# Performance work log

Measured on AMD Instinct MI355X. Metric: run time of the kernel, lower is better.

The kernel has to match this reference:

```python
import jax, jax.numpy as jnp
import numpy as np

S1 = (42, 1600, 1408); S2 = (21, 800, 704); S3 = (11, 400, 352); S4 = (6, 200, 176)
OFF = np.array([[dz, dy, dx] for dz in (-1, 0, 1) for dy in (-1, 0, 1) for dx in (-1, 0, 1)], np.int64)
KOFF = np.array([[kz, ky, kx] for kz in (0, 1, 2) for ky in (0, 1, 2) for kx in (0, 1, 2)], np.int64)

def _keys(c, s):
    return (c[:, 0] * s[1] + c[:, 1]) * s[2] + c[:, 2]

def _lookup(skeys, qk, valid):
    pos = np.searchsorted(skeys, qk)
    posc = np.clip(pos, 0, len(skeys) - 1)
    found = valid & (skeys[posc] == qk)
    return np.where(found, posc, -1).astype(np.int32)

def _subm_nbr(coords, skeys, shape):
    N = len(coords); nbr = np.empty((N, 27), np.int32); sh = np.array(shape)
    for t in range(27):
        q = coords + OFF[t]
        valid = np.all((q >= 0) & (q < sh), axis=1)
        nbr[:, t] = _lookup(skeys, _keys(q, shape), valid)
    return nbr

def _inv_nbr(fcoords, ckeys, cshape):
    # inverse of stride-2, pad-1, k-3 sparse conv: coarse = (fine + 1 - k) / 2
    N = len(fcoords); nbr = np.empty((N, 27), np.int32); csh = np.array(cshape)
    for t in range(27):
        cand = fcoords + 1 - KOFF[t]
        valid = np.all(cand >= 0, axis=1) & np.all(cand % 2 == 0, axis=1)
        cc = cand // 2
        valid &= np.all(cc < csh, axis=1)
        nbr[:, t] = _lookup(ckeys, _keys(cc, cshape), valid)
    return nbr

def _geometry():
    rng = np.random.default_rng(0)
    n = 130000
    c = np.stack([rng.integers(0, S1[i], n) for i in range(3)], 1).astype(np.int64)
    uk, idx = np.unique(_keys(c, S1), return_index=True)
    c1 = c[idx][:100000]; k1 = uk[:len(c1)]
    def down(cf, s):
        cc = cf // 2
        uk, idx = np.unique(_keys(cc, s), return_index=True)
        return cc[idx], uk
    c2, k2 = down(c1, S2); c3, k3 = down(c2, S3); c4, k4 = down(c3, S4)
    return dict(nbr4=_subm_nbr(c4, k4, S4), inv43=_inv_nbr(c3, k4, S4),
                nbr3=_subm_nbr(c3, k3, S3), inv32=_inv_nbr(c2, k3, S3),
                nbr2=_subm_nbr(c2, k2, S2), inv21=_inv_nbr(c1, k2, S2),
                nbr1=_subm_nbr(c1, k1, S1), n4=len(c4), n1=len(c1))

_SPECS = [("m4", 64, 64), ("i4", 64, 64), ("m3", 64, 64), ("i3", 64, 32),
          ("m2", 32, 32), ("i2", 32, 16), ("m1", 16, 16), ("c5", 16, 3)]

def _params(key):
    p = {}
    for i, (nm, ci, co) in enumerate(_SPECS):
        k = jax.random.fold_in(key, i)
        p["W_" + nm] = jax.random.normal(k, (27, ci, co), jnp.float32) * (1.0 / np.sqrt(27.0 * ci))
        p["g_" + nm] = jnp.ones((co,), jnp.float32)
        p["b_" + nm] = jnp.zeros((co,), jnp.float32)
    return p

def setup_inputs() -> dict:
    geo = _geometry()
    key = jax.random.key(0)
    inp = {k: jnp.asarray(v) for k, v in geo.items() if k.startswith(("nbr", "inv"))}
    inp["x"] = jax.random.normal(jax.random.fold_in(key, 100), (geo["n4"], 64), jnp.float32)
    inp.update(_params(key))
    return inp

def _block(f, nbr, W, g, b, relu=True):
    # gather-GEMM (sparse conv), then BatchNorm1d (training mode, eps=1e-3), then ReLU
    m = nbr >= 0                                             # [N,27]
    x = jnp.where(m[..., None], f[jnp.maximum(nbr, 0)], 0.0)  # [N,27,Cin]
    y = jnp.einsum('nkc,kcd->nd', x, W)                      # [N,Cout]
    mu = y.mean(0); var = y.var(0)
    y = (y - mu) * jax.lax.rsqrt(var + 1e-3) * g + b
    return jax.nn.relu(y) if relu else y

def reference(x, nbr4, inv43, nbr3, inv32, nbr2, inv21, nbr1,
              W_m4, g_m4, b_m4, W_i4, g_i4, b_i4, W_m3, g_m3, b_m3, W_i3, g_i3, b_i3,
              W_m2, g_m2, b_m2, W_i2, g_i2, b_i2, W_m1, g_m1, b_m1, W_c5, g_c5, b_c5):
    h = _block(x, nbr4, W_m4, g_m4, b_m4)      # subm4: [N4,64]
    h = _block(h, inv43, W_i4, g_i4, b_i4)     # inverse conv4 -> [N3,64]
    h = _block(h, nbr3, W_m3, g_m3, b_m3)      # subm3
    h = _block(h, inv32, W_i3, g_i3, b_i3)     # inverse conv3 -> [N2,32]
    h = _block(h, nbr2, W_m2, g_m2, b_m2)      # subm2
    h = _block(h, inv21, W_i2, g_i2, b_i2)     # inverse conv2 -> [N1,16]
    h = _block(h, nbr1, W_m1, g_m1, b_m1)      # subm1
    return _block(h, nbr1, W_c5, g_c5, b_c5, relu=False)  # conv5 (shares subm1 rulebook), BN only
```

## Files before the change

kernel.cpp:

```cpp
#include <hip/hip_runtime.h>

typedef _Float16 HALF;
typedef _Float16 f16x8 __attribute__((ext_vector_type(8)));
typedef float f32x4 __attribute__((ext_vector_type(4)));
typedef int i32x4 __attribute__((ext_vector_type(4)));

struct WArgs { const float* W[8]; HALF* dst[8]; };

__global__ void convert_all_w_kernel(WArgs a)
{
    const int CIs[8]  = {64, 64, 64, 64, 32, 32, 16, 16};
    const int COs[8]  = {64, 64, 64, 32, 32, 16, 16, 3};
    const int COPs[8] = {64, 64, 64, 32, 32, 16, 16, 16};
    const int L = blockIdx.y;
    const int CI = CIs[L], CO = COs[L], COP = COPs[L];
    const int K = 27 * CI, KP = (K + 31) & ~31;
    const int total = COP * KP;
    for (int i = blockIdx.x * 256 + threadIdx.x; i < total; i += gridDim.x * 256) {
        int jp = i / KP;
        int kp = i - jp * KP;
        float v = (jp < CO && kp < K) ? a.W[L][(size_t)kp * CO + jp] : 0.f;
        a.dst[L][((size_t)(kp >> 5) * COP + jp) * 32 + (kp & 31)] = (HALF)v;
    }
}

__global__ void convert_x_kernel(const float* __restrict__ x, HALF* __restrict__ xh, int total)
{
    int i = blockIdx.x * 256 + threadIdx.x;
    if (i < total) xh[i] = (HALF)x[i];
}

template<int CI, int CO_PAD, int NMT, bool FUSED>
__global__ __launch_bounds__(256, 2) void conv_kernel(
    const HALF* __restrict__ h, const int* __restrict__ nbr,
    const HALF* __restrict__ Wt, HALF* __restrict__ yout,
    float* __restrict__ sums, int n,
    const float* __restrict__ psums, const float* __restrict__ pg,
    const float* __restrict__ pb, float pinvn)
{
    constexpr int K    = 27 * CI;
    constexpr int KP   = (K + 31) & ~31;
    constexpr int NCH  = KP / 32;
    constexpr int NJB  = CO_PAD / 16;
    constexpr int NW   = 4;
    constexpr int NCB  = (CI >= 64) ? 2 : 1;
    constexpr int LOG2CI = (CI == 64) ? 6 : ((CI == 32) ? 5 : 4);

    __shared__ float red[2][NW][CO_PAD];

    const int wv   = threadIdx.x >> 6;
    const int lane = threadIdx.x & 63;
    const int l15  = lane & 15;
    const int lq   = lane >> 4;

    int bid = blockIdx.x;
    {
        const int nwg = gridDim.x;
        const int q = nwg >> 3, r = nwg & 7;
        const int xcd = bid & 7, idx = bid >> 3;
        bid = (xcd < r ? xcd * (q + 1) : r * (q + 1) + (xcd - r) * q) + idx;
    }
    const int waveRow = bid * (NW * 16 * NMT) + wv * (16 * NMT);

    f32x4 acc[NMT][NJB];
#pragma unroll
    for (int mt = 0; mt < NMT; ++mt)
#pragma unroll
        for (int jb = 0; jb < NJB; ++jb)
#pragma unroll
            for (int r = 0; r < 4; ++r) acc[mt][jb][r] = 0.f;

    int  nbo[NMT];
    bool rok[NMT];
#pragma unroll
    for (int mt = 0; mt < NMT; ++mt) {
        const int row = waveRow + mt * 16 + l15;
        rok[mt] = row < n;
        nbo[mt] = min(row, n - 1) * 27;
    }

    f16x8 sc8[NCB], bi8[NCB];
    if constexpr (FUSED) {
#pragma unroll
        for (int cb = 0; cb < NCB; ++cb) {
            const int c0 = cb * 32 + ((lq * 8) & (CI - 1));
#pragma unroll
            for (int j = 0; j < 8; ++j) {
                const int c = c0 + j;
                const float mu  = psums[c] * pinvn;
                const float var = psums[CI + c] * pinvn - mu * mu;
                const float sc  = rsqrtf(var + 1e-3f) * pg[c];
                sc8[cb][j] = (HALF)sc;
                bi8[cb][j] = (HALF)(pb[c] - mu * sc);
            }
        }
    }

    #define TAPOF(kc) ((CI == 16) ? (2 * (kc) + (lq >> 1)) : ((CI == 64) ? ((kc) >> 1) : (kc)))
    #define CHOF(kc)  (((kc) * 32 + lq * 8) & (CI - 1))

    int   ipf[2][NMT];
    f16x8 apf[2][NMT];
#pragma unroll
    for (int p = 0; p < 2; ++p) {
#pragma unroll
        for (int mt = 0; mt < NMT; ++mt) {
            const int t   = TAPOF(p);
            const int v   = nbr[nbo[mt] + (t < 27 ? t : 26)];
            const int idx = (rok[mt] && t < 27) ? v : -1;
            ipf[p][mt] = idx;
            apf[p][mt] = *(const f16x8*)(h + ((max(idx, 0) << LOG2CI) + CHOF(p)));
        }
    }

#pragma unroll
    for (int kc = 0; kc < NCH; ++kc) {
        const int cur = kc & 1;
        const int ccb = (NCB == 2) ? (kc & 1) : 0;

        const HALF* wb = Wt + (size_t)kc * (CO_PAD * 32) + lq * 8;
        f16x8 b[NJB];
#pragma unroll
        for (int jb = 0; jb < NJB; ++jb)
            b[jb] = *(const f16x8*)(wb + (size_t)(jb * 16 + l15) * 32);

        f16x8 a_use[NMT];
        int   i_use[NMT];
#pragma unroll
        for (int mt = 0; mt < NMT; ++mt) { a_use[mt] = apf[cur][mt]; i_use[mt] = ipf[cur][mt]; }

        if (kc + 2 < NCH) {
#pragma unroll
            for (int mt = 0; mt < NMT; ++mt) {
                const int t   = TAPOF(kc + 2);
                const int v   = nbr[nbo[mt] + (t < 27 ? t : 26)];
                const int idx = (rok[mt] && t < 27) ? v : -1;
                ipf[cur][mt] = idx;
                apf[cur][mt] = *(const f16x8*)(h + ((max(idx, 0) << LOG2CI) + CHOF(kc + 2)));
            }
        }

#pragma unroll
        for (int mt = 0; mt < NMT; ++mt) {
            f16x8 a = a_use[mt];
            if constexpr (FUSED) {
                a = a * sc8[ccb] + bi8[ccb];
#pragma unroll
                for (int j = 0; j < 8; ++j)
                    a[j] = (a[j] < (HALF)0.f) ? (HALF)0.f : a[j];
            }
            const int m = ~(i_use[mt] >> 31);
            i32x4 ai = __builtin_bit_cast(i32x4, a);
            ai.x &= m; ai.y &= m; ai.z &= m; ai.w &= m;
            a = __builtin_bit_cast(f16x8, ai);
#pragma unroll
            for (int jb = 0; jb < NJB; ++jb)
                acc[mt][jb] = __builtin_amdgcn_mfma_f32_16x16x32_f16(a, b[jb], acc[mt][jb], 0, 0, 0);
        }
    }
    #undef TAPOF
    #undef CHOF

#pragma unroll
    for (int jb = 0; jb < NJB; ++jb) {
        const int col = jb * 16 + l15;
        float s = 0.f, sq = 0.f;
#pragma unroll
        for (int mt = 0; mt < NMT; ++mt) {
            const int rb = waveRow + mt * 16 + lq * 4;
#pragma unroll
            for (int r = 0; r < 4; ++r) {
                if (rb + r < n) {
                    const float v = acc[mt][jb][r];
                    yout[(size_t)(rb + r) * CO_PAD + col] = (HALF)v;
                    s += v;
                    sq += v * v;
                }
            }
        }
        s  += __shfl_xor(s, 16);  s  += __shfl_xor(s, 32);
        sq += __shfl_xor(sq, 16); sq += __shfl_xor(sq, 32);
        if (lane < 16) { red[0][wv][col] = s; red[1][wv][col] = sq; }
    }
    __syncthreads();
    if (threadIdx.x < CO_PAD) {
        float s = 0.f, sq = 0.f;
#pragma unroll
        for (int w = 0; w < NW; ++w) { s += red[0][w][threadIdx.x]; sq += red[1][w][threadIdx.x]; }
        atomicAdd(&sums[threadIdx.x], s);
        atomicAdd(&sums[CO_PAD + threadIdx.x], sq);
    }
}

__global__ void bn_out_kernel(const HALF* __restrict__ y, const float* __restrict__ sums,
                              const float* __restrict__ g, const float* __restrict__ b,
                              int n, float invn, float* __restrict__ out)
{
    int i = blockIdx.x * 256 + threadIdx.x;
    if (i >= n * 3) return;
    int row = i / 3;
    int c = i - row * 3;
    float mu  = sums[c] * invn;
    float var = sums[16 + c] * invn - mu * mu;
    float sc  = rsqrtf(var + 1e-3f) * g[c];
    out[i] = ((float)y[(size_t)row * 16 + c] - mu) * sc + b[c];
}

extern "C" void kernel_launch(void* const* d_in, const int* in_sizes, int n_in,
                              void* d_out, int out_size, void* d_ws, size_t ws_size,
                              hipStream_t stream)
{
    const int* nbr4  = (const int*)d_in[0];
    const int* inv43 = (const int*)d_in[1];
    const int* nbr3  = (const int*)d_in[2];
    const int* inv32 = (const int*)d_in[3];
    const int* nbr2  = (const int*)d_in[4];
    const int* inv21 = (const int*)d_in[5];
    const int* nbr1  = (const int*)d_in[6];
    const float* x   = (const float*)d_in[7];

    const int n4 = in_sizes[0] / 27;
    const int n3 = in_sizes[1] / 27;
    const int n2 = in_sizes[3] / 27;
    const int n1 = in_sizes[5] / 27;

    const int CIs[8]  = {64, 64, 64, 64, 32, 32, 16, 16};
    const int COPs[8] = {64, 64, 64, 32, 32, 16, 16, 16};
    int KPs[8], wtoff[8];
    int wtot = 0;
    for (int s = 0; s < 8; ++s) {
        KPs[s] = ((27 * CIs[s] + 31) / 32) * 32;
        wtoff[s] = wtot;
        wtot += COPs[s] * KPs[s];
    }

    char* ws = (char*)d_ws;
    HALF* wt = (HALF*)ws;
    size_t off = ((size_t)wtot * sizeof(HALF) + 255) & ~(size_t)255;
    float* sums = (float*)(ws + off);
    off += 8 * 128 * sizeof(float);
    off = (off + 255) & ~(size_t)255;
    HALF* xh = (HALF*)(ws + off);
    off += ((size_t)n4 * 64 * sizeof(HALF) + 255) & ~(size_t)255;
    size_t bufElems = 0;
    {
        size_t cand[4] = {(size_t)n4 * 64, (size_t)n3 * 64, (size_t)n2 * 32, (size_t)n1 * 16};
        for (int i = 0; i < 4; ++i) if (cand[i] > bufElems) bufElems = cand[i];
    }
    HALF* Y0 = (HALF*)(ws + off);
    off += (bufElems * sizeof(HALF) + 255) & ~(size_t)255;
    HALF* Y1 = (HALF*)(ws + off);

    hipMemsetAsync(sums, 0, 8 * 128 * sizeof(float), stream);

    WArgs wa;
    for (int s = 0; s < 8; ++s) { wa.W[s] = (const float*)d_in[8 + 3 * s]; wa.dst[s] = wt + wtoff[s]; }
    {
        int maxTotal = 64 * KPs[0];
        dim3 grid((maxTotal + 255) / 256, 8);
        convert_all_w_kernel<<<grid, 256, 0, stream>>>(wa);
    }
    convert_x_kernel<<<(n4 * 64 + 255) / 256, 256, 0, stream>>>(x, xh, n4 * 64);

#define G(s) ((const float*)d_in[9 + 3 * (s)])
#define B(s) ((const float*)d_in[10 + 3 * (s)])
#define SUMS(s) (sums + (s) * 128)
#define GRID(nn) (((nn) + 127) / 128)

    conv_kernel<64, 64, 2, false><<<GRID(n4), 256, 0, stream>>>(
        xh, nbr4, wt + wtoff[0], Y0, SUMS(0), n4, nullptr, nullptr, nullptr, 0.f);
    conv_kernel<64, 64, 2, true><<<GRID(n3), 256, 0, stream>>>(
        Y0, inv43, wt + wtoff[1], Y1, SUMS(1), n3, SUMS(0), G(0), B(0), 1.f / n4);
    conv_kernel<64, 64, 2, true><<<GRID(n3), 256, 0, stream>>>(
        Y1, nbr3, wt + wtoff[2], Y0, SUMS(2), n3, SUMS(1), G(1), B(1), 1.f / n3);
    conv_kernel<64, 32, 2, true><<<GRID(n2), 256, 0, stream>>>(
        Y0, inv32, wt + wtoff[3], Y1, SUMS(3), n2, SUMS(2), G(2), B(2), 1.f / n3);
    conv_kernel<32, 32, 2, true><<<GRID(n2), 256, 0, stream>>>(
        Y1, nbr2, wt + wtoff[4], Y0, SUMS(4), n2, SUMS(3), G(3), B(3), 1.f / n2);
    conv_kernel<32, 16, 2, true><<<GRID(n1), 256, 0, stream>>>(
        Y0, inv21, wt + wtoff[5], Y1, SUMS(5), n1, SUMS(4), G(4), B(4), 1.f / n2);
    conv_kernel<16, 16, 2, true><<<GRID(n1), 256, 0, stream>>>(
        Y1, nbr1, wt + wtoff[6], Y0, SUMS(6), n1, SUMS(5), G(5), B(5), 1.f / n1);
    conv_kernel<16, 16, 2, true><<<GRID(n1), 256, 0, stream>>>(
        Y0, nbr1, wt + wtoff[7], Y1, SUMS(7), n1, SUMS(6), G(6), B(6), 1.f / n1);
    bn_out_kernel<<<(n1 * 3 + 255) / 256, 256, 0, stream>>>(
        Y1, SUMS(7), G(7), B(7), n1, 1.f / n1, (float*)d_out);

#undef G
#undef B
#undef SUMS
#undef GRID
}
```

Measured before the change: 568.1 us.

## Split K reduction across waves and shard BN stat atomics per XCD

Each block now covers 32 rows instead of 128. Its four waves each take a quarter of the K chunks for the same rows, and the partial accumulators are combined through a tree reduction in shared memory before wave 0 writes the output and statistics. The BN sums are spread across 8 slices chosen by XCD, so atomics contend less, and consumers add up the 8 slices when they compute mean and variance. This raises the number of blocks and the parallelism per row at the cost of extra LDS traffic, three barriers, and reloading weights four times more often.

```diff
diff --git a/kernel.cpp b/kernel.cpp
--- a/kernel.cpp
+++ b/kernel.cpp
@@ -43,10 +43,14 @@
     constexpr int NCH  = KP / 32;
     constexpr int NJB  = CO_PAD / 16;
     constexpr int NW   = 4;
+    constexpr int CHK  = (NCH + NW - 1) / NW;
     constexpr int NCB  = (CI >= 64) ? 2 : 1;
+    static_assert(NCB == 1 || (CHK & 1) == 0, "sc8 parity must stay compile-time");
     constexpr int LOG2CI = (CI == 64) ? 6 : ((CI == 32) ? 5 : 4);
-
-    __shared__ float red[2][NW][CO_PAD];
+    constexpr int ROWS  = 16 * NMT;
+    constexpr int PAIRS = NMT * NJB;
+
+    __shared__ f32x4 lred[2][PAIRS * 64];
 
     const int wv   = threadIdx.x >> 6;
     const int lane = threadIdx.x & 63;
@@ -60,7 +64,7 @@
         const int xcd = bid & 7, idx = bid >> 3;
         bid = (xcd < r ? xcd * (q + 1) : r * (q + 1) + (xcd - r) * q) + idx;
     }
-    const int waveRow = bid * (NW * 16 * NMT) + wv * (16 * NMT);
+    const int rowBase = bid * ROWS;
 
     f32x4 acc[NMT][NJB];
 #pragma unroll
@@ -74,7 +78,7 @@
     bool rok[NMT];
 #pragma unroll
     for (int mt = 0; mt < NMT; ++mt) {
-        const int row = waveRow + mt * 16 + l15;
+        const int row = rowBase + mt * 16 + l15;
         rok[mt] = row < n;
         nbo[mt] = min(row, n - 1) * 27;
     }
@@ -87,8 +91,14 @@
 #pragma unroll
             for (int j = 0; j < 8; ++j) {
                 const int c = c0 + j;
-                const float mu  = psums[c] * pinvn;
-                const float var = psums[CI + c] * pinvn - mu * mu;
+                float ssum = 0.f, qsum = 0.f;
+#pragma unroll
+                for (int k2 = 0; k2 < 8; ++k2) {
+                    ssum += psums[k2 * 128 + c];
+                    qsum += psums[k2 * 128 + CI + c];
+                }
+                const float mu  = ssum * pinvn;
+                const float var = qsum * pinvn - mu * mu;
                 const float sc  = rsqrtf(var + 1e-3f) * pg[c];
                 sc8[cb][j] = (HALF)sc;
                 bi8[cb][j] = (HALF)(pb[c] - mu * sc);
@@ -96,27 +106,32 @@
         }
     }
 
-    #define TAPOF(kc) ((CI == 16) ? (2 * (kc) + (lq >> 1)) : ((CI == 64) ? ((kc) >> 1) : (kc)))
-    #define CHOF(kc)  (((kc) * 32 + lq * 8) & (CI - 1))
+    #define TAPOF(kc_) ((CI == 16) ? (2 * (kc_) + (lq >> 1)) : ((CI == 64) ? ((kc_) >> 1) : (kc_)))
+    #define CHOF(kc_)  ((((kc_) * 32) + lq * 8) & (CI - 1))
+
+    const int kc0 = wv * CHK;
 
     int   ipf[2][NMT];
     f16x8 apf[2][NMT];
 #pragma unroll
     for (int p = 0; p < 2; ++p) {
+        const int kc = kc0 + p;
 #pragma unroll
         for (int mt = 0; mt < NMT; ++mt) {
-            const int t   = TAPOF(p);
+            const int t   = TAPOF(kc);
             const int v   = nbr[nbo[mt] + (t < 27 ? t : 26)];
             const int idx = (rok[mt] && t < 27) ? v : -1;
             ipf[p][mt] = idx;
-            apf[p][mt] = *(const f16x8*)(h + ((max(idx, 0) << LOG2CI) + CHOF(p)));
-        }
-    }
-
-#pragma unroll
-    for (int kc = 0; kc < NCH; ++kc) {
-        const int cur = kc & 1;
-        const int ccb = (NCB == 2) ? (kc & 1) : 0;
+            apf[p][mt] = *(const f16x8*)(h + ((max(idx, 0) << LOG2CI) + CHOF(kc)));
+        }
+    }
+
+#pragma unroll
+    for (int kc2 = 0; kc2 < CHK; ++kc2) {
+        const int kc = kc0 + kc2;
+        if (kc >= NCH) break;
+        const int cur = kc2 & 1;
+        const int ccb = (NCB == 2) ? (kc2 & 1) : 0;
 
         const HALF* wb = Wt + (size_t)kc * (CO_PAD * 32) + lq * 8;
         f16x8 b[NJB];
@@ -129,7 +144,7 @@
 #pragma unroll
         for (int mt = 0; mt < NMT; ++mt) { a_use[mt] = apf[cur][mt]; i_use[mt] = ipf[cur][mt]; }
 
-        if (kc + 2 < NCH) {
+        if (kc2 + 2 < CHK && kc + 2 < NCH) {
 #pragma unroll
             for (int mt = 0; mt < NMT; ++mt) {
                 const int t   = TAPOF(kc + 2);
@@ -161,34 +176,63 @@
     #undef TAPOF
     #undef CHOF
 
-#pragma unroll
-    for (int jb = 0; jb < NJB; ++jb) {
-        const int col = jb * 16 + l15;
-        float s = 0.f, sq = 0.f;
-#pragma unroll
-        for (int mt = 0; mt < NMT; ++mt) {
-            const int rb = waveRow + mt * 16 + lq * 4;
-#pragma unroll
-            for (int r = 0; r < 4; ++r) {
-                if (rb + r < n) {
-                    const float v = acc[mt][jb][r];
-                    yout[(size_t)(rb + r) * CO_PAD + col] = (HALF)v;
-                    s += v;
-                    sq += v * v;
+    if (wv & 1) {
+#pragma unroll
+        for (int mt = 0; mt < NMT; ++mt)
+#pragma unroll
+            for (int jb = 0; jb < NJB; ++jb)
+                lred[wv >> 1][(mt * NJB + jb) * 64 + lane] = acc[mt][jb];
+    }
+    __syncthreads();
+    if (!(wv & 1)) {
+#pragma unroll
+        for (int mt = 0; mt < NMT; ++mt)
+#pragma unroll
+            for (int jb = 0; jb < NJB; ++jb)
+                acc[mt][jb] += lred[wv >> 1][(mt * NJB + jb) * 64 + lane];
+    }
+    __syncthreads();
+    if (wv == 2) {
+#pragma unroll
+        for (int mt = 0; mt < NMT; ++mt)
+#pragma unroll
+            for (int jb = 0; jb < NJB; ++jb)
+                lred[0][(mt * NJB + jb) * 64 + lane] = acc[mt][jb];
+    }
+    __syncthreads();
+
+    if (wv == 0) {
+#pragma unroll
+        for (int mt = 0; mt < NMT; ++mt)
+#pragma unroll
+            for (int jb = 0; jb < NJB; ++jb)
+                acc[mt][jb] += lred[0][(mt * NJB + jb) * 64 + lane];
+
+        float* sl = sums + (bid & 7) * 128;
+#pragma unroll
+        for (int jb = 0; jb < NJB; ++jb) {
+            const int col = jb * 16 + l15;
+            float s = 0.f, sq = 0.f;
+#pragma unroll
+            for (int mt = 0; mt < NMT; ++mt) {
+                const int rb = rowBase + mt * 16 + lq * 4;
+#pragma unroll
+                for (int r = 0; r < 4; ++r) {
+                    if (rb + r < n) {
+                        const float v = acc[mt][jb][r];
+                        yout[(size_t)(rb + r) * CO_PAD + col] = (HALF)v;
+                        s += v;
+                        sq += v * v;
+                    }
                 }
             }
-        }
-        s  += __shfl_xor(s, 16);  s  += __shfl_xor(s, 32);
-        sq += __shfl_xor(sq, 16); sq += __shfl_xor(sq, 32);
-        if (lane < 16) { red[0][wv][col] = s; red[1][wv][col] = sq; }
-    }
-    __syncthreads();
-    if (threadIdx.x < CO_PAD) {
-        float s = 0.f, sq = 0.f;
-#pragma unroll
-        for (int w = 0; w < NW; ++w) { s += red[0][w][threadIdx.x]; sq += red[1][w][threadIdx.x]; }
-        atomicAdd(&sums[threadIdx.x], s);
-        atomicAdd(&sums[CO_PAD + threadIdx.x], sq);
+            s  += __shfl_xor(s, 16);  s  += __shfl_xor(s, 32);
+            sq += __shfl_xor(sq, 16); sq += __shfl_xor(sq, 32);
+            if (lane < 16) {
+                atomicAdd(&sl[col], s);
+                atomicAdd(&sl[CO_PAD + col], sq);
+            }
+        }
     }
 }
 
@@ -200,8 +244,14 @@
     if (i >= n * 3) return;
     int row = i / 3;
     int c = i - row * 3;
-    float mu  = sums[c] * invn;
-    float var = sums[16 + c] * invn - mu * mu;
+    float ssum = 0.f, qsum = 0.f;
+#pragma unroll
+    for (int k2 = 0; k2 < 8; ++k2) {
+        ssum += sums[k2 * 128 + c];
+        qsum += sums[k2 * 128 + 16 + c];
+    }
+    float mu  = ssum * invn;
+    float var = qsum * invn - mu * mu;
     float sc  = rsqrtf(var + 1e-3f) * g[c];
     out[i] = ((float)y[(size_t)row * 16 + c] - mu) * sc + b[c];
 }
@@ -238,7 +288,7 @@
     HALF* wt = (HALF*)ws;
     size_t off = ((size_t)wtot * sizeof(HALF) + 255) & ~(size_t)255;
     float* sums = (float*)(ws + off);
-    off += 8 * 128 * sizeof(float);
+    off += 8 * 1024 * sizeof(float);
     off = (off + 255) & ~(size_t)255;
     HALF* xh = (HALF*)(ws + off);
     off += ((size_t)n4 * 64 * sizeof(HALF) + 255) & ~(size_t)255;
@@ -251,7 +301,7 @@
     off += (bufElems * sizeof(HALF) + 255) & ~(size_t)255;
     HALF* Y1 = (HALF*)(ws + off);
 
-    hipMemsetAsync(sums, 0, 8 * 128 * sizeof(float), stream);
+    hipMemsetAsync(sums, 0, 8 * 1024 * sizeof(float), stream);
 
     WArgs wa;
     for (int s = 0; s < 8; ++s) { wa.W[s] = (const float*)d_in[8 + 3 * s]; wa.dst[s] = wt + wtoff[s]; }
@@ -264,8 +314,8 @@
 
 #define G(s) ((const float*)d_in[9 + 3 * (s)])
 #define B(s) ((const float*)d_in[10 + 3 * (s)])
-#define SUMS(s) (sums + (s) * 128)
-#define GRID(nn) (((nn) + 127) / 128)
+#define SUMS(s) (sums + (s) * 1024)
+#define GRID(nn) (((nn) + 31) / 32)
 
     conv_kernel<64, 64, 2, false><<<GRID(n4), 256, 0, stream>>>(
         xh, nbr4, wt + wtoff[0], Y0, SUMS(0), n4, nullptr, nullptr, nullptr, 0.f);
```

Measured after the change: 642.0 us. 1.13x slower.
